# Kernel optimization log

Measured on AMD Instinct MI355X. Metric: run time of the kernel, lower is better.

The kernel has to match this reference:

```python
import jax, jax.numpy as jnp
import numpy as np

LORA_ALPHA = 16.0
TOP_K = 2


def setup_inputs() -> dict:
    key = jax.random.key(0)
    k_x, k_w, k_g, k_a, k_b = jax.random.split(key, 5)
    B, S, H, O, E, R = 2, 2048, 2048, 2048, 8, 16
    x = jax.random.normal(k_x, (B, S, H), dtype=jnp.float32)
    weight = jax.random.normal(k_w, (O, H), dtype=jnp.float32)          # frozen base W [out, in]
    gate_w = jax.random.normal(k_g, (E, H), dtype=jnp.float32) * 0.02   # router gate [E, in]
    A_w = jax.random.normal(k_a, (E, R, H), dtype=jnp.float32) * (1.0 / np.sqrt(H))  # stacked lora_A
    B_w = jax.random.normal(k_b, (E, O, R), dtype=jnp.float32) * 0.01   # stacked lora_B
    return {"x": x, "weight": weight, "gate_w": gate_w, "A_w": A_w, "B_w": B_w}


def reference(x, weight, gate_w, A_w, B_w):
    E = gate_w.shape[0]
    # Base frozen linear: F.linear(x, weight)
    out = jnp.einsum("bsh,oh->bso", x, weight)

    # Router: softmax over experts, top-2, renormalize
    logits = jnp.einsum("bsh,eh->bse", x, gate_w)
    probs = jax.nn.softmax(logits, axis=-1)
    topk_w, topk_idx = jax.lax.top_k(probs, TOP_K)          # [b,s,2]
    topk_w = topk_w / jnp.sum(topk_w, axis=-1, keepdims=True)

    # Per-token combine weight for each expert (sum over the 2 slots)
    onehot = jax.nn.one_hot(topk_idx, E, dtype=x.dtype)      # [b,s,2,E]
    cw = jnp.einsum("bsk,bske->bse", topk_w, onehot)         # [b,s,E]

    # LoRA: down-project into all experts' rank spaces, weight, then up-project.
    # t: [b,s,E,r] is small (r=16); weighting here avoids a [b,s,E,out] buffer.
    t = jnp.einsum("bsh,erh->bser", x, A_w)
    t = t * cw[..., None]
    lora = jnp.einsum("bser,eor->bso", t, B_w)

    return out + LORA_ALPHA * lora
```

## Files before the change

### kernel.cpp

```cpp
#include <hip/hip_runtime.h>
#include <hip/hip_bf16.h>


typedef __bf16 bf16x8 __attribute__((ext_vector_type(8)));
typedef float f32x4 __attribute__((ext_vector_type(4)));

__device__ __forceinline__ __bf16 f2bf(float f) { return (__bf16)f; }

__device__ __forceinline__ void ld_lds16(const void* g, void* l) {
  __builtin_amdgcn_global_load_lds((__attribute__((address_space(1))) void*)g,
                                   (__attribute__((address_space(3))) void*)l,
                                   16, 0, 0);
}

__global__ void prep_kernel(const float* __restrict__ W, const float* __restrict__ Aw,
                            const float* __restrict__ Bw, __bf16* __restrict__ Bfull,
                            __bf16* __restrict__ A2) {
  const int b = blockIdx.x, tid = threadIdx.x;
  if (b < 2176) {
    const float* src = (b < 2048) ? (W + (size_t)b * 2048)
                                  : (Aw + (size_t)(b - 2048) * 2048);
    __bf16* dst = (b < 2048) ? (Bfull + (size_t)b * 2176)
                             : (A2 + (size_t)(b - 2048) * 2048);
    const int c = tid * 8;
    float4 a = *(const float4*)(src + c);
    float4 d = *(const float4*)(src + c + 4);
    bf16x8 v;
    v[0] = f2bf(a.x); v[1] = f2bf(a.y); v[2] = f2bf(a.z); v[3] = f2bf(a.w);
    v[4] = f2bf(d.x); v[5] = f2bf(d.y); v[6] = f2bf(d.z); v[7] = f2bf(d.w);
    *(bf16x8*)(dst + c) = v;
  } else {
    const int idx = (b - 2176) * 256 + tid;
    const int e = idx >> 11, o = idx & 2047;
    const float4* s = (const float4*)(Bw + ((size_t)e * 2048 + o) * 16);
    float4 v0 = s[0], v1 = s[1], v2 = s[2], v3 = s[3];
    __bf16* d = Bfull + (size_t)o * 2176 + 2048 + e * 16;
    bf16x8 lo, hi;
    lo[0] = f2bf(v0.x); lo[1] = f2bf(v0.y); lo[2] = f2bf(v0.z); lo[3] = f2bf(v0.w);
    lo[4] = f2bf(v1.x); lo[5] = f2bf(v1.y); lo[6] = f2bf(v1.z); lo[7] = f2bf(v1.w);
    hi[0] = f2bf(v2.x); hi[1] = f2bf(v2.y); hi[2] = f2bf(v2.z); hi[3] = f2bf(v2.w);
    hi[4] = f2bf(v3.x); hi[5] = f2bf(v3.y); hi[6] = f2bf(v3.z); hi[7] = f2bf(v3.w);
    *(bf16x8*)d = lo;
    *(bf16x8*)(d + 8) = hi;
  }
}

__global__ __launch_bounds__(512) void router_t2(
    const float* __restrict__ x, const float* __restrict__ gw,
    const __bf16* __restrict__ A2, __bf16* __restrict__ Abuf) {
  __shared__ __align__(16) __bf16 xs[16][2056];
  __shared__ float red[8][16][8];
  __shared__ float cws[16][8];
  const int tid = threadIdx.x;
  const int wave = tid >> 6, lane = tid & 63;
  const int t0 = blockIdx.x * 16;

  {
    const int half = tid >> 8;
    const int tid2 = tid & 255;
#pragma unroll 4
    for (int i2 = 0; i2 < 8; ++i2) {
      const int i = i2 * 2 + half;
      const float* xr = x + (size_t)(t0 + i) * 2048 + tid2 * 8;
      float4 a = *(const float4*)xr;
      float4 b = *(const float4*)(xr + 4);
      bf16x8 v;
      v[0] = f2bf(a.x); v[1] = f2bf(a.y); v[2] = f2bf(a.z); v[3] = f2bf(a.w);
      v[4] = f2bf(b.x); v[5] = f2bf(b.y); v[6] = f2bf(b.z); v[7] = f2bf(b.w);
      *(bf16x8*)(Abuf + (size_t)(t0 + i) * 2176 + tid2 * 8) = v;
      *(bf16x8*)&xs[i][tid2 * 8] = v;
    }
  }
  __syncthreads();

  const int tok = tid & 15, slc = tid >> 4;
  const int c0 = slc * 64;
  float acc[8] = {0, 0, 0, 0, 0, 0, 0, 0};
  for (int j8 = 0; j8 < 8; ++j8) {
    bf16x8 xv = *(const bf16x8*)&xs[tok][c0 + j8 * 8];
    float xf[8];
#pragma unroll
    for (int j = 0; j < 8; ++j) xf[j] = (float)xv[j];
#pragma unroll
    for (int e = 0; e < 8; ++e) {
      float4 g0 = *(const float4*)(gw + e * 2048 + c0 + j8 * 8);
      float4 g1 = *(const float4*)(gw + e * 2048 + c0 + j8 * 8 + 4);
      acc[e] += xf[0] * g0.x + xf[1] * g0.y + xf[2] * g0.z + xf[3] * g0.w +
                xf[4] * g1.x + xf[5] * g1.y + xf[6] * g1.z + xf[7] * g1.w;
    }
  }
#pragma unroll
  for (int e = 0; e < 8; ++e) {
    acc[e] += __shfl_down(acc[e], 16);
    acc[e] += __shfl_down(acc[e], 32);
  }
  if (lane < 16) {
#pragma unroll
    for (int e = 0; e < 8; ++e) red[wave][lane][e] = acc[e];
  }
  __syncthreads();
  if (tid < 16) {
    float lg[8];
#pragma unroll
    for (int e = 0; e < 8; ++e)
      lg[e] = red[0][tid][e] + red[1][tid][e] + red[2][tid][e] + red[3][tid][e] +
              red[4][tid][e] + red[5][tid][e] + red[6][tid][e] + red[7][tid][e];
    int a = 0;
    for (int e = 1; e < 8; ++e) if (lg[e] > lg[a]) a = e;
    int b = (a == 0) ? 1 : 0;
    for (int e = 0; e < 8; ++e) if (e != a && lg[e] > lg[b]) b = e;
    const float d = __expf(lg[b] - lg[a]);
    float o[8] = {0, 0, 0, 0, 0, 0, 0, 0};
    o[a] = 1.0f / (1.0f + d);
    o[b] = d / (1.0f + d);
#pragma unroll
    for (int e = 0; e < 8; ++e) cws[tid][e] = o[e];
  }
  __syncthreads();

  const int m = lane & 15, q = lane >> 4;
  const int nt = wave;
  f32x4 tacc = {};
  for (int ks = 0; ks < 64; ++ks) {
    bf16x8 af = *(const bf16x8*)&xs[m][ks * 32 + q * 8];
    bf16x8 bfg = *(const bf16x8*)(A2 + (size_t)(nt * 16 + m) * 2048 +
                                  ks * 32 + q * 8);
    tacc = __builtin_amdgcn_mfma_f32_16x16x32_bf16(af, bfg, tacc, 0, 0, 0);
  }
#pragma unroll
  for (int rg = 0; rg < 4; ++rg) {
    const int trow = q * 4 + rg;
    const float s = tacc[rg] * 16.0f * cws[trow][nt];
    Abuf[(size_t)(t0 + trow) * 2176 + 2048 + nt * 16 + m] = f2bf(s);
  }
}

__global__ __launch_bounds__(256, 2) void mfma_gemm_bt4(
    const __bf16* __restrict__ A, const __bf16* __restrict__ B,
    float* __restrict__ C, int lda, int ldb, int ldc, int kiters) {
  __shared__ __align__(16) __bf16 lds[2 * 16384];
  const int tid = threadIdx.x;
  const int wave = tid >> 6;
  const int lane = tid & 63;

  const int wg = blockIdx.x + (blockIdx.y << 5);
  const int xcd = wg & 7, loc = wg >> 3;
  const int tm = ((xcd & 3) * 8 + (loc >> 3)) * 128;
  const int tn = ((xcd >> 2) * 8 + (loc & 7)) * 128;

  const int srow = lane >> 3;
  const int skoff = ((lane & 7) ^ srow) * 8;

  const int wr = wave >> 1, wc = wave & 1;
  const int rlo = lane & 7;
  const int rb3 = (lane >> 3) & 1;
  const int qb = lane >> 4;

  f32x4 acc[4][4] = {};

  auto stage = [&](int buf, int kt) {
    const int kc = kt * 64;
    __bf16* Ls = lds + buf * 16384;
#pragma unroll
    for (int r = 0; r < 4; ++r) {
      const int ch = wave + r * 4;
      ld_lds16(A + (size_t)(tm + ch * 8 + srow) * lda + kc + skoff, &Ls[ch * 512]);
    }
#pragma unroll
    for (int r = 0; r < 4; ++r) {
      const int ch = wave + r * 4;
      ld_lds16(B + (size_t)(tn + ch * 8 + srow) * ldb + kc + skoff,
               &Ls[8192 + ch * 512]);
    }
  };

  stage(0, 0);

  for (int kt = 0; kt < kiters; ++kt) {
    const int cb = kt & 1;
    if (kt + 1 < kiters) {
      stage(cb ^ 1, kt + 1);
      asm volatile("s_waitcnt vmcnt(8)" ::: "memory");
    } else {
      asm volatile("s_waitcnt vmcnt(0)" ::: "memory");
    }
    __builtin_amdgcn_s_barrier();

    const __bf16* As = lds + cb * 16384;
    const __bf16* Bs = As + 8192;
#pragma unroll
    for (int ks = 0; ks < 2; ++ks) {
      bf16x8 af[4], bfg[4];
      const int q8 = ((ks * 4 + qb) ^ rlo) * 8;
#pragma unroll
      for (int i = 0; i < 4; ++i) {
        const int rh = wr * 8 + i * 2 + rb3;
        af[i] = *(const bf16x8*)&As[rh * 512 + rlo * 64 + q8];
      }
#pragma unroll
      for (int j = 0; j < 4; ++j) {
        const int rh = wc * 8 + j * 2 + rb3;
        bfg[j] = *(const bf16x8*)&Bs[rh * 512 + rlo * 64 + q8];
      }
      __builtin_amdgcn_s_setprio(1);
#pragma unroll
      for (int i = 0; i < 4; ++i)
#pragma unroll
        for (int j = 0; j < 4; ++j)
          acc[i][j] =
              __builtin_amdgcn_mfma_f32_16x16x32_bf16(af[i], bfg[j], acc[i][j], 0, 0, 0);
      __builtin_amdgcn_s_setprio(0);
    }
    __builtin_amdgcn_s_barrier();
  }

  const int crow0 = tm + wr * 64 + (lane >> 4) * 4;
  const int ccol0 = tn + wc * 64 + (lane & 15);
#pragma unroll
  for (int i = 0; i < 4; ++i)
#pragma unroll
    for (int j = 0; j < 4; ++j)
#pragma unroll
      for (int rg = 0; rg < 4; ++rg)
        C[(size_t)(crow0 + i * 16 + rg) * ldc + ccol0 + j * 16] = acc[i][j][rg];
}

extern "C" void kernel_launch(void* const* d_in, const int* in_sizes, int n_in,
                              void* d_out, int out_size, void* d_ws, size_t ws_size,
                              hipStream_t stream) {
  const float* x = (const float*)d_in[0];
  const float* weight = (const float*)d_in[1];
  const float* gate_w = (const float*)d_in[2];
  const float* A_w = (const float*)d_in[3];
  const float* B_w = (const float*)d_in[4];
  float* out = (float*)d_out;

  char* ws = (char*)d_ws;
  __bf16* Abuf = (__bf16*)ws;
  __bf16* Bfull = (__bf16*)(ws + 17825792);
  __bf16* A2 = (__bf16*)(ws + 26738688);

  prep_kernel<<<2240, 256, 0, stream>>>(weight, A_w, B_w, Bfull, A2);
  router_t2<<<256, 512, 0, stream>>>(x, gate_w, A2, Abuf);
  mfma_gemm_bt4<<<dim3(32, 16), 256, 0, stream>>>(Abuf, Bfull, out, 2176, 2176,
                                                  2048, 34);
}
```

Before: 158.8 us.

## Fuse weight conversion into router kernel, split out small A-weight prep

```diff
diff --git a/kernel.cpp b/kernel.cpp
--- a/kernel.cpp
+++ b/kernel.cpp
@@ -13,47 +13,61 @@
                                    16, 0, 0);
 }
 
-__global__ void prep_kernel(const float* __restrict__ W, const float* __restrict__ Aw,
-                            const float* __restrict__ Bw, __bf16* __restrict__ Bfull,
-                            __bf16* __restrict__ A2) {
-  const int b = blockIdx.x, tid = threadIdx.x;
-  if (b < 2176) {
-    const float* src = (b < 2048) ? (W + (size_t)b * 2048)
-                                  : (Aw + (size_t)(b - 2048) * 2048);
-    __bf16* dst = (b < 2048) ? (Bfull + (size_t)b * 2176)
-                             : (A2 + (size_t)(b - 2048) * 2048);
-    const int c = tid * 8;
-    float4 a = *(const float4*)(src + c);
-    float4 d = *(const float4*)(src + c + 4);
-    bf16x8 v;
-    v[0] = f2bf(a.x); v[1] = f2bf(a.y); v[2] = f2bf(a.z); v[3] = f2bf(a.w);
-    v[4] = f2bf(d.x); v[5] = f2bf(d.y); v[6] = f2bf(d.z); v[7] = f2bf(d.w);
-    *(bf16x8*)(dst + c) = v;
-  } else {
-    const int idx = (b - 2176) * 256 + tid;
-    const int e = idx >> 11, o = idx & 2047;
-    const float4* s = (const float4*)(Bw + ((size_t)e * 2048 + o) * 16);
-    float4 v0 = s[0], v1 = s[1], v2 = s[2], v3 = s[3];
-    __bf16* d = Bfull + (size_t)o * 2176 + 2048 + e * 16;
-    bf16x8 lo, hi;
-    lo[0] = f2bf(v0.x); lo[1] = f2bf(v0.y); lo[2] = f2bf(v0.z); lo[3] = f2bf(v0.w);
-    lo[4] = f2bf(v1.x); lo[5] = f2bf(v1.y); lo[6] = f2bf(v1.z); lo[7] = f2bf(v1.w);
-    hi[0] = f2bf(v2.x); hi[1] = f2bf(v2.y); hi[2] = f2bf(v2.z); hi[3] = f2bf(v2.w);
-    hi[4] = f2bf(v3.x); hi[5] = f2bf(v3.y); hi[6] = f2bf(v3.z); hi[7] = f2bf(v3.w);
-    *(bf16x8*)d = lo;
-    *(bf16x8*)(d + 8) = hi;
-  }
-}
-
-__global__ __launch_bounds__(512) void router_t2(
+__global__ __launch_bounds__(256) void a2_prep(const float* __restrict__ Aw,
+                                               __bf16* __restrict__ A2) {
+  const int row = blockIdx.x;
+  const int c = threadIdx.x * 8;
+  const float* src = Aw + (size_t)row * 2048 + c;
+  float4 a = *(const float4*)src;
+  float4 d = *(const float4*)(src + 4);
+  bf16x8 v;
+  v[0] = f2bf(a.x); v[1] = f2bf(a.y); v[2] = f2bf(a.z); v[3] = f2bf(a.w);
+  v[4] = f2bf(d.x); v[5] = f2bf(d.y); v[6] = f2bf(d.z); v[7] = f2bf(d.w);
+  *(bf16x8*)(A2 + (size_t)row * 2048 + c) = v;
+}
+
+__global__ __launch_bounds__(512) void fused_pre(
     const float* __restrict__ x, const float* __restrict__ gw,
-    const __bf16* __restrict__ A2, __bf16* __restrict__ Abuf) {
+    const __bf16* __restrict__ A2, const float* __restrict__ W,
+    const float* __restrict__ Bw, __bf16* __restrict__ Abuf,
+    __bf16* __restrict__ Bfull) {
   __shared__ __align__(16) __bf16 xs[16][2056];
   __shared__ float red[8][16][8];
   __shared__ float cws[16][8];
+  const int b = blockIdx.x;
   const int tid = threadIdx.x;
+
+  if (b >= 256) {
+    const int pb = b - 256;
+    if (pb < 1024) {
+      const int row = pb * 2 + (tid >> 8);
+      const int c = (tid & 255) * 8;
+      const float* src = W + (size_t)row * 2048 + c;
+      float4 a = *(const float4*)src;
+      float4 d = *(const float4*)(src + 4);
+      bf16x8 v;
+      v[0] = f2bf(a.x); v[1] = f2bf(a.y); v[2] = f2bf(a.z); v[3] = f2bf(a.w);
+      v[4] = f2bf(d.x); v[5] = f2bf(d.y); v[6] = f2bf(d.z); v[7] = f2bf(d.w);
+      *(bf16x8*)(Bfull + (size_t)row * 2176 + c) = v;
+    } else {
+      const int idx = (pb - 1024) * 512 + tid;
+      const int e = idx >> 11, o = idx & 2047;
+      const float4* s = (const float4*)(Bw + ((size_t)e * 2048 + o) * 16);
+      float4 v0 = s[0], v1 = s[1], v2 = s[2], v3 = s[3];
+      __bf16* d = Bfull + (size_t)o * 2176 + 2048 + e * 16;
+      bf16x8 lo, hi;
+      lo[0] = f2bf(v0.x); lo[1] = f2bf(v0.y); lo[2] = f2bf(v0.z); lo[3] = f2bf(v0.w);
+      lo[4] = f2bf(v1.x); lo[5] = f2bf(v1.y); lo[6] = f2bf(v1.z); lo[7] = f2bf(v1.w);
+      hi[0] = f2bf(v2.x); hi[1] = f2bf(v2.y); hi[2] = f2bf(v2.z); hi[3] = f2bf(v2.w);
+      hi[4] = f2bf(v3.x); hi[5] = f2bf(v3.y); hi[6] = f2bf(v3.z); hi[7] = f2bf(v3.w);
+      *(bf16x8*)d = lo;
+      *(bf16x8*)(d + 8) = hi;
+    }
+    return;
+  }
+
   const int wave = tid >> 6, lane = tid & 63;
-  const int t0 = blockIdx.x * 16;
+  const int t0 = b * 16;
 
   {
     const int half = tid >> 8;
@@ -63,10 +77,10 @@
       const int i = i2 * 2 + half;
       const float* xr = x + (size_t)(t0 + i) * 2048 + tid2 * 8;
       float4 a = *(const float4*)xr;
-      float4 b = *(const float4*)(xr + 4);
+      float4 bb = *(const float4*)(xr + 4);
       bf16x8 v;
       v[0] = f2bf(a.x); v[1] = f2bf(a.y); v[2] = f2bf(a.z); v[3] = f2bf(a.w);
-      v[4] = f2bf(b.x); v[5] = f2bf(b.y); v[6] = f2bf(b.z); v[7] = f2bf(b.w);
+      v[4] = f2bf(bb.x); v[5] = f2bf(bb.y); v[6] = f2bf(bb.z); v[7] = f2bf(bb.w);
       *(bf16x8*)(Abuf + (size_t)(t0 + i) * 2176 + tid2 * 8) = v;
       *(bf16x8*)&xs[i][tid2 * 8] = v;
     }
@@ -107,12 +121,12 @@
               red[4][tid][e] + red[5][tid][e] + red[6][tid][e] + red[7][tid][e];
     int a = 0;
     for (int e = 1; e < 8; ++e) if (lg[e] > lg[a]) a = e;
-    int b = (a == 0) ? 1 : 0;
-    for (int e = 0; e < 8; ++e) if (e != a && lg[e] > lg[b]) b = e;
-    const float d = __expf(lg[b] - lg[a]);
+    int bb = (a == 0) ? 1 : 0;
+    for (int e = 0; e < 8; ++e) if (e != a && lg[e] > lg[bb]) bb = e;
+    const float d = __expf(lg[bb] - lg[a]);
     float o[8] = {0, 0, 0, 0, 0, 0, 0, 0};
     o[a] = 1.0f / (1.0f + d);
-    o[b] = d / (1.0f + d);
+    o[bb] = d / (1.0f + d);
 #pragma unroll
     for (int e = 0; e < 8; ++e) cws[tid][e] = o[e];
   }
@@ -240,8 +254,8 @@
   __bf16* Bfull = (__bf16*)(ws + 17825792);
   __bf16* A2 = (__bf16*)(ws + 26738688);
 
-  prep_kernel<<<2240, 256, 0, stream>>>(weight, A_w, B_w, Bfull, A2);
-  router_t2<<<256, 512, 0, stream>>>(x, gate_w, A2, Abuf);
+  a2_prep<<<128, 256, 0, stream>>>(A_w, A2);
+  fused_pre<<<1312, 512, 0, stream>>>(x, gate_w, A2, weight, B_w, Abuf, Bfull);
   mfma_gemm_bt4<<<dim3(32, 16), 256, 0, stream>>>(Abuf, Bfull, out, 2176, 2176,
                                                   2048, 34);
 }
```

Result: no change. 161.5 us (+1.7%).

## Split router kernel waves into concurrent gate and LoRA-A projection roles

Applied to the files above, without the earlier changes.

```diff
diff --git a/kernel.cpp b/kernel.cpp
--- a/kernel.cpp
+++ b/kernel.cpp
@@ -49,7 +49,6 @@
     const float* __restrict__ x, const float* __restrict__ gw,
     const __bf16* __restrict__ A2, __bf16* __restrict__ Abuf) {
   __shared__ __align__(16) __bf16 xs[16][2056];
-  __shared__ float red[8][16][8];
   __shared__ float cws[16][8];
   const int tid = threadIdx.x;
   const int wave = tid >> 6, lane = tid & 63;
@@ -73,65 +72,73 @@
   }
   __syncthreads();
 
-  const int tok = tid & 15, slc = tid >> 4;
-  const int c0 = slc * 64;
-  float acc[8] = {0, 0, 0, 0, 0, 0, 0, 0};
-  for (int j8 = 0; j8 < 8; ++j8) {
-    bf16x8 xv = *(const bf16x8*)&xs[tok][c0 + j8 * 8];
-    float xf[8];
-#pragma unroll
-    for (int j = 0; j < 8; ++j) xf[j] = (float)xv[j];
+  const int m = lane & 15, q = lane >> 4;
+  f32x4 tacc[2] = {};
+
+  if (wave < 4) {
+    const int tg = lane >> 4;
+    const int tok = wave * 4 + tg;
+    const int slc = lane & 15;
+    const int c0 = slc * 128;
+    float acc[8] = {0, 0, 0, 0, 0, 0, 0, 0};
+    for (int j8 = 0; j8 < 16; ++j8) {
+      bf16x8 xv = *(const bf16x8*)&xs[tok][c0 + j8 * 8];
+      float xf[8];
+#pragma unroll
+      for (int j = 0; j < 8; ++j) xf[j] = (float)xv[j];
+#pragma unroll
+      for (int e = 0; e < 8; ++e) {
+        float4 g0 = *(const float4*)(gw + e * 2048 + c0 + j8 * 8);
+        float4 g1 = *(const float4*)(gw + e * 2048 + c0 + j8 * 8 + 4);
+        acc[e] += xf[0] * g0.x + xf[1] * g0.y + xf[2] * g0.z + xf[3] * g0.w +
+                  xf[4] * g1.x + xf[5] * g1.y + xf[6] * g1.z + xf[7] * g1.w;
+      }
+    }
 #pragma unroll
     for (int e = 0; e < 8; ++e) {
-      float4 g0 = *(const float4*)(gw + e * 2048 + c0 + j8 * 8);
-      float4 g1 = *(const float4*)(gw + e * 2048 + c0 + j8 * 8 + 4);
-      acc[e] += xf[0] * g0.x + xf[1] * g0.y + xf[2] * g0.z + xf[3] * g0.w +
-                xf[4] * g1.x + xf[5] * g1.y + xf[6] * g1.z + xf[7] * g1.w;
-    }
-  }
-#pragma unroll
-  for (int e = 0; e < 8; ++e) {
-    acc[e] += __shfl_down(acc[e], 16);
-    acc[e] += __shfl_down(acc[e], 32);
-  }
-  if (lane < 16) {
-#pragma unroll
-    for (int e = 0; e < 8; ++e) red[wave][lane][e] = acc[e];
+      acc[e] += __shfl_xor(acc[e], 8);
+      acc[e] += __shfl_xor(acc[e], 4);
+      acc[e] += __shfl_xor(acc[e], 2);
+      acc[e] += __shfl_xor(acc[e], 1);
+    }
+    if (slc == 0) {
+      int a_ = 0;
+      for (int e = 1; e < 8; ++e) if (acc[e] > acc[a_]) a_ = e;
+      int b_ = (a_ == 0) ? 1 : 0;
+      for (int e = 0; e < 8; ++e) if (e != a_ && acc[e] > acc[b_]) b_ = e;
+      const float d = __expf(acc[b_] - acc[a_]);
+      float o[8] = {0, 0, 0, 0, 0, 0, 0, 0};
+      o[a_] = 1.0f / (1.0f + d);
+      o[b_] = d / (1.0f + d);
+#pragma unroll
+      for (int e = 0; e < 8; ++e) cws[tok][e] = o[e];
+    }
+  } else {
+    const int nt0 = (wave - 4) * 2;
+    for (int ks = 0; ks < 64; ++ks) {
+      bf16x8 af = *(const bf16x8*)&xs[m][ks * 32 + q * 8];
+#pragma unroll
+      for (int h = 0; h < 2; ++h) {
+        bf16x8 bfg = *(const bf16x8*)(A2 + (size_t)((nt0 + h) * 16 + m) * 2048 +
+                                      ks * 32 + q * 8);
+        tacc[h] = __builtin_amdgcn_mfma_f32_16x16x32_bf16(af, bfg, tacc[h], 0, 0, 0);
+      }
+    }
   }
   __syncthreads();
-  if (tid < 16) {
-    float lg[8];
-#pragma unroll
-    for (int e = 0; e < 8; ++e)
-      lg[e] = red[0][tid][e] + red[1][tid][e] + red[2][tid][e] + red[3][tid][e] +
-              red[4][tid][e] + red[5][tid][e] + red[6][tid][e] + red[7][tid][e];
-    int a = 0;
-    for (int e = 1; e < 8; ++e) if (lg[e] > lg[a]) a = e;
-    int b = (a == 0) ? 1 : 0;
-    for (int e = 0; e < 8; ++e) if (e != a && lg[e] > lg[b]) b = e;
-    const float d = __expf(lg[b] - lg[a]);
-    float o[8] = {0, 0, 0, 0, 0, 0, 0, 0};
-    o[a] = 1.0f / (1.0f + d);
-    o[b] = d / (1.0f + d);
-#pragma unroll
-    for (int e = 0; e < 8; ++e) cws[tid][e] = o[e];
-  }
-  __syncthreads();
-
-  const int m = lane & 15, q = lane >> 4;
-  const int nt = wave;
-  f32x4 tacc = {};
-  for (int ks = 0; ks < 64; ++ks) {
-    bf16x8 af = *(const bf16x8*)&xs[m][ks * 32 + q * 8];
-    bf16x8 bfg = *(const bf16x8*)(A2 + (size_t)(nt * 16 + m) * 2048 +
-                                  ks * 32 + q * 8);
-    tacc = __builtin_amdgcn_mfma_f32_16x16x32_bf16(af, bfg, tacc, 0, 0, 0);
-  }
-#pragma unroll
-  for (int rg = 0; rg < 4; ++rg) {
-    const int trow = q * 4 + rg;
-    const float s = tacc[rg] * 16.0f * cws[trow][nt];
-    Abuf[(size_t)(t0 + trow) * 2176 + 2048 + nt * 16 + m] = f2bf(s);
+
+  if (wave >= 4) {
+    const int nt0 = (wave - 4) * 2;
+#pragma unroll
+    for (int h = 0; h < 2; ++h) {
+      const int nt = nt0 + h;
+#pragma unroll
+      for (int rg = 0; rg < 4; ++rg) {
+        const int trow = q * 4 + rg;
+        const float s = tacc[h][rg] * 16.0f * cws[trow][nt];
+        Abuf[(size_t)(t0 + trow) * 2176 + 2048 + nt * 16 + m] = f2bf(s);
+      }
+    }
   }
 }
 
```

After: 178.4 us. 12.3% more time.
